# Optimization experiments

Measured on AMD Instinct MI355X. Metric: run time of the kernel, lower is better.

The kernel has to match this reference:

```python
import math
import jax, jax.numpy as jnp
import numpy as np

SEQ_LEN = 512
NUM_HEADS = 16
HEAD_DIM = 64  # hidden_size // num_heads
MAX_REL = 127


def _relative_positions_embeddings(length, depth, max_relative_position=MAX_REL):
    """Sinusoidal table gathered by clipped relative distance -> [L, L, depth]."""
    vocab = 2 * max_relative_position + 1
    pos = np.arange(vocab, dtype=np.float64)[:, None]
    i = np.arange(depth // 2, dtype=np.float64)[None, :]
    angle = pos / np.power(10000.0, 2.0 * i / depth)
    table = np.zeros((vocab, depth), dtype=np.float64)
    table[:, 0::2] = np.sin(angle)
    table[:, 1::2] = np.cos(angle)
    r = np.arange(length)
    dist = np.clip(r[None, :] - r[:, None], -max_relative_position, max_relative_position)
    final = dist + max_relative_position  # [L, L] indices into vocab
    return jnp.asarray(table[final], dtype=jnp.float32)  # [L, L, depth]

_REL_EMB = _relative_positions_embeddings(SEQ_LEN, HEAD_DIM)


def setup_inputs() -> dict:
    key = jax.random.key(0)
    ks = jax.random.split(key, 4)
    B, S, H = 8, SEQ_LEN, NUM_HEADS * HEAD_DIM
    scale = 1.0 / math.sqrt(H)
    return {
        "hidden_states": jax.random.normal(ks[0], (B, S, H), dtype=jnp.float32),
        "attention_mask": jnp.zeros((B, 1, 1, S), dtype=jnp.float32),
        "Wq": jax.random.normal(ks[1], (H, H), dtype=jnp.float32) * scale,
        "bq": jnp.zeros((H,), dtype=jnp.float32),
        "Wk": jax.random.normal(ks[2], (H, H), dtype=jnp.float32) * scale,
        "bk": jnp.zeros((H,), dtype=jnp.float32),
        "Wv": jax.random.normal(ks[3], (H, H), dtype=jnp.float32) * scale,
        "bv": jnp.zeros((H,), dtype=jnp.float32),
    }


def reference(hidden_states, attention_mask, Wq, bq, Wk, bk, Wv, bv):
    B, S, _ = hidden_states.shape
    H, D = NUM_HEADS, HEAD_DIM

    def split_heads(x):  # [B,S,H*D] -> [B,H,S,D]
        return x.reshape(B, S, H, D).transpose(0, 2, 1, 3)

    q = split_heads(hidden_states @ Wq.T + bq)
    k = split_heads(hidden_states @ Wk.T + bk)
    v = split_heads(hidden_states @ Wv.T + bv)

    rel = _REL_EMB[:S, :S, :]  # [S, S, D]

    scores = jnp.einsum("bhqd,bhkd->bhqk", q, k)
    scores = scores + jnp.einsum("bhqd,qkd->bhqk", q, rel)
    scores = scores / math.sqrt(D) + attention_mask

    probs = jax.nn.softmax(scores, axis=-1)  # dropout prob = 0.0 (eval)

    ctx = jnp.einsum("bhqk,bhkd->bhqd", probs, v)
    ctx = ctx + jnp.einsum("bhqk,qkd->bhqd", probs, rel)

    context_layer = ctx.transpose(0, 2, 1, 3).reshape(B, S, H * D)
    return context_layer, scores
```

## Files before the change

### kernel.cpp

```cpp
#include <hip/hip_runtime.h>
#include <hip/hip_bf16.h>

typedef __attribute__((ext_vector_type(4))) float f32x4;
typedef __attribute__((ext_vector_type(8))) short bf16x8;

#define NB 8
#define NS 512
#define NH 16
#define ND 64
#define HID 1024
#define NBH (NB*NH)
#define NROWS (NB*NS)

static __device__ __forceinline__ ushort f2bf(float x){
    union{float f; unsigned u;} a; a.f = x;
    unsigned r = a.u + 0x7fffu + ((a.u >> 16) & 1u);
    return (ushort)(r >> 16);
}
static __device__ __forceinline__ float bf2f(ushort x){
    union{unsigned u; float f;} a; a.u = ((unsigned)x) << 16;
    return a.f;
}

__global__ void build_tables(ushort* __restrict__ tab, ushort* __restrict__ tabT){
    int t = blockIdx.x * blockDim.x + threadIdx.x;
    if (t >= 256 * 64) return;
    int p = t >> 6, d = t & 63;
    float val = 0.f;
    if (p < 255){
        int i = d >> 1;
        float angle = (float)p / powf(10000.f, (float)i / 32.f);
        val = (d & 1) ? cosf(angle) : sinf(angle);
    }
    ushort b = f2bf(val);
    tab[p * 64 + d]  = b;
    tabT[d * 256 + p] = b;
}

__global__ void cvt_bf16(const float* __restrict__ src, ushort* __restrict__ dst, int n4){
    int i = blockIdx.x * blockDim.x + threadIdx.x;
    if (i >= n4) return;
    float4 v = reinterpret_cast<const float4*>(src)[i];
    ushort4 o;
    o.x = f2bf(v.x); o.y = f2bf(v.y); o.z = f2bf(v.z); o.w = f2bf(v.w);
    reinterpret_cast<ushort4*>(dst)[i] = o;
}

__global__ void cvt_bf16_w3(const float* __restrict__ w0, const float* __restrict__ w1,
                            const float* __restrict__ w2, ushort* __restrict__ o0,
                            ushort* __restrict__ o1, ushort* __restrict__ o2, int n4){
    int i = blockIdx.x * blockDim.x + threadIdx.x;
    if (i >= n4) return;
    const float* src = blockIdx.y == 0 ? w0 : (blockIdx.y == 1 ? w1 : w2);
    ushort* dst      = blockIdx.y == 0 ? o0 : (blockIdx.y == 1 ? o1 : o2);
    float4 v = reinterpret_cast<const float4*>(src)[i];
    ushort4 o;
    o.x = f2bf(v.x); o.y = f2bf(v.y); o.z = f2bf(v.z); o.w = f2bf(v.w);
    reinterpret_cast<ushort4*>(dst)[i] = o;
}

__global__ __launch_bounds__(256) void proj_gemm_qkv(
    const ushort* __restrict__ X,
    const ushort* __restrict__ Wqp, const ushort* __restrict__ Wkp, const ushort* __restrict__ Wvp,
    const float* __restrict__ bqp, const float* __restrict__ bkp, const float* __restrict__ bvp,
    ushort* __restrict__ outQ, ushort* __restrict__ outK, ushort* __restrict__ outV)
{
    __shared__ ushort lA[128][72];
    __shared__ ushort lB[128][72];
    int sel = blockIdx.x >> 3;
    const ushort* W   = sel == 0 ? Wqp : (sel == 1 ? Wkp : Wvp);
    const float* bias = sel == 0 ? bqp : (sel == 1 ? bkp : bvp);
    ushort* out       = sel == 0 ? outQ : (sel == 1 ? outK : outV);
    int n0 = (blockIdx.x & 7) * 128;
    int m0 = blockIdx.y * 128;
    int tid = threadIdx.x;
    int wave = tid >> 6, lane = tid & 63;
    int wr = (wave >> 1) * 64, wc = (wave & 1) * 64;
    int lrow = lane & 15, lk8 = (lane >> 4) * 8;

    f32x4 acc[4][4] = {};

    for (int k0 = 0; k0 < HID; k0 += 64){
        __syncthreads();
        #pragma unroll
        for (int i = 0; i < 4; ++i){
            int chunk = i * 256 + tid;
            int row = chunk >> 3, col = (chunk & 7) * 8;
            *reinterpret_cast<uint4*>(&lA[row][col]) =
                *reinterpret_cast<const uint4*>(&X[(size_t)(m0 + row) * HID + k0 + col]);
            *reinterpret_cast<uint4*>(&lB[row][col]) =
                *reinterpret_cast<const uint4*>(&W[(size_t)(n0 + row) * HID + k0 + col]);
        }
        __syncthreads();
        #pragma unroll
        for (int ks = 0; ks < 2; ++ks){
            bf16x8 af[4], bfr[4];
            #pragma unroll
            for (int m = 0; m < 4; ++m)
                af[m] = *reinterpret_cast<const bf16x8*>(&lA[wr + m*16 + lrow][ks*32 + lk8]);
            #pragma unroll
            for (int n = 0; n < 4; ++n)
                bfr[n] = *reinterpret_cast<const bf16x8*>(&lB[wc + n*16 + lrow][ks*32 + lk8]);
            #pragma unroll
            for (int m = 0; m < 4; ++m)
                #pragma unroll
                for (int n = 0; n < 4; ++n)
                    acc[m][n] = __builtin_amdgcn_mfma_f32_16x16x32_bf16(af[m], bfr[n], acc[m][n], 0, 0, 0);
        }
    }

    #pragma unroll
    for (int m = 0; m < 4; ++m){
        #pragma unroll
        for (int n = 0; n < 4; ++n){
            int col = n0 + wc + n*16 + lrow;
            float bv = bias[col];
            int h = col >> 6, d = col & 63;
            #pragma unroll
            for (int r = 0; r < 4; ++r){
                int mg = m0 + wr + m*16 + (lane >> 4)*4 + r;
                int b = mg >> 9, s = mg & 511;
                float val = acc[m][n][r] + bv;
                if (sel != 2)
                    out[(((size_t)(b*NH + h))*NS + s)*ND + d] = f2bf(val);
                else
                    out[(((size_t)(b*NH + h))*ND + d)*NS + s] = f2bf(val);
            }
        }
    }
}

__global__ __launch_bounds__(256, 6) void fused_attn(
    const ushort* __restrict__ Qb, const ushort* __restrict__ Kb,
    const ushort* __restrict__ vT, const ushort* __restrict__ tab,
    const ushort* __restrict__ tabT, const float* __restrict__ mask,
    float* __restrict__ scores, float* __restrict__ ctx)
{
    __shared__ ushort pL[16][512];
    __shared__ ushort qq[16][256];
    __shared__ float  rsum[16][4];
    __shared__ float  rleft[16][4];
    __shared__ float  rright[16][4];
    ushort* pLf = &pL[0][0];
    ushort* qqf = &qq[0][0];
#define SWZ(row, col) ((col) ^ (((row)&7)<<3))

    const int bh = blockIdx.x;
    const int b = bh >> 4, h = bh & 15;
    const int q0 = blockIdx.y * 16;
    const int wave = threadIdx.x >> 6, lane = threadIdx.x & 63;
    const int lrow = lane & 15, g = lane >> 4, lk8 = g * 8;

    const ushort* Qh = Qb + (size_t)bh * NS * ND;
    const ushort* Kh = Kb + (size_t)bh * NS * ND;
    const int q = q0 + lrow;

    bf16x8 qf0 = *reinterpret_cast<const bf16x8*>(&Qh[(size_t)(q0 + lrow)*ND + lk8]);
    bf16x8 qf1 = *reinterpret_cast<const bf16x8*>(&Qh[(size_t)(q0 + lrow)*ND + 32 + lk8]);

    #pragma unroll
    for (int t = 0; t < 4; ++t){
        const ushort* src = &tab[(size_t)(wave*64 + t*16 + lrow)*ND];
        bf16x8 k0v = *reinterpret_cast<const bf16x8*>(&src[lk8]);
        bf16x8 k1v = *reinterpret_cast<const bf16x8*>(&src[32 + lk8]);
        f32x4 at = __builtin_amdgcn_mfma_f32_16x16x32_bf16(k0v, qf0, (f32x4){0.f,0.f,0.f,0.f}, 0, 0, 0);
        at = __builtin_amdgcn_mfma_f32_16x16x32_bf16(k1v, qf1, at, 0, 0, 0);
        ushort4 w;
        w.x = f2bf(at[0]); w.y = f2bf(at[1]); w.z = f2bf(at[2]); w.w = f2bf(at[3]);
        int col = wave*64 + t*16 + g*4;
        *reinterpret_cast<ushort4*>(&qqf[lrow*256 + SWZ(lrow, col)]) = w;
    }
    __syncthreads();

    float st = 0.f, sl = 0.f, sr = 0.f;
    const float* maskb = &mask[b*NS];
    float* srow = &scores[((size_t)bh*NS + q)*NS];
    const ushort* srcK0 = &Kh[(size_t)(wave*128 + lrow)*ND];
    bf16x8 ka = *reinterpret_cast<const bf16x8*>(&srcK0[lk8]);
    bf16x8 kb = *reinterpret_cast<const bf16x8*>(&srcK0[32 + lk8]);
    #pragma unroll
    for (int n = 0; n < 8; ++n){
        bf16x8 ka1, kb1;
        if (n < 7){
            const ushort* s1 = &Kh[(size_t)(wave*128 + (n+1)*16 + lrow)*ND];
            ka1 = *reinterpret_cast<const bf16x8*>(&s1[lk8]);
            kb1 = *reinterpret_cast<const bf16x8*>(&s1[32 + lk8]);
        }
        int kbase = wave*128 + n*16 + g*4;
        f32x4 a = __builtin_amdgcn_mfma_f32_16x16x32_bf16(ka, qf0, (f32x4){0.f,0.f,0.f,0.f}, 0, 0, 0);
        a = __builtin_amdgcn_mfma_f32_16x16x32_bf16(kb, qf1, a, 0, 0, 0);
        float4 mk4 = *reinterpret_cast<const float4*>(&maskb[kbase]);
        float mk[4] = {mk4.x, mk4.y, mk4.z, mk4.w};
        f32x4 sv;
        ushort4 pw;
        #pragma unroll
        for (int r = 0; r < 4; ++r){
            int k = kbase + r;
            int dd = min(127, max(-127, k - q));
            float val = (a[r] + bf2f(qqf[lrow*256 + SWZ(lrow, dd + 127)])) * 0.125f + mk[r];
            sv[r] = val;
            float e = __expf(val);
            st += e;
            if (k <= q - 127) sl += e;
            if (k >= q + 127) sr += e;
            ((ushort*)&pw)[r] = f2bf(e);
        }
        *reinterpret_cast<f32x4*>(&srow[kbase]) = sv;
        *reinterpret_cast<ushort4*>(&pLf[lrow*512 + SWZ(lrow, kbase)]) = pw;
        ka = ka1; kb = kb1;
    }
    st += __shfl_xor(st, 16); st += __shfl_xor(st, 32);
    sl += __shfl_xor(sl, 16); sl += __shfl_xor(sl, 32);
    sr += __shfl_xor(sr, 16); sr += __shfl_xor(sr, 32);
    if (lane < 16){
        rsum[lrow][wave]   = st;
        rleft[lrow][wave]  = sl;
        rright[lrow][wave] = sr;
    }
    __syncthreads();

    if (wave == 0 && lane < 16){
        float SL = rleft[lrow][0] + rleft[lrow][1] + rleft[lrow][2] + rleft[lrow][3];
        float SR = rright[lrow][0] + rright[lrow][1] + rright[lrow][2] + rright[lrow][3];
        qqf[lrow*256 + SWZ(lrow, 0)]   = f2bf(SL);
        qqf[lrow*256 + SWZ(lrow, 254)] = f2bf(SR);
    }
    for (int idx = threadIdx.x; idx < 16*256; idx += 256){
        int row = idx >> 8, j = idx & 255;
        if (j == 0 || j >= 254) continue;
        int col = q0 + row + j - 127;
        qqf[row*256 + SWZ(row, j)] =
            (col >= 0 && col < NS) ? pLf[row*512 + SWZ(row, col)] : (ushort)0;
    }
    __syncthreads();

    const int d = wave*16 + lrow;
    const ushort* vTh = vT + ((size_t)bh*ND + d)*NS;
    const ushort* tTd = tabT + (size_t)d*256;
    f32x4 o0 = (f32x4){0.f,0.f,0.f,0.f};
    f32x4 o1 = (f32x4){0.f,0.f,0.f,0.f};
    __builtin_amdgcn_s_setprio(1);
    #pragma unroll
    for (int k0 = 0; k0 < NS; k0 += 64){
        bf16x8 bv0 = *reinterpret_cast<const bf16x8*>(&vTh[k0 + lk8]);
        bf16x8 pa0 = *reinterpret_cast<const bf16x8*>(&pLf[lrow*512 + SWZ(lrow, k0 + lk8)]);
        o0 = __builtin_amdgcn_mfma_f32_16x16x32_bf16(pa0, bv0, o0, 0, 0, 0);
        bf16x8 bv1 = *reinterpret_cast<const bf16x8*>(&vTh[k0 + 32 + lk8]);
        bf16x8 pa1 = *reinterpret_cast<const bf16x8*>(&pLf[lrow*512 + SWZ(lrow, k0 + 32 + lk8)]);
        o1 = __builtin_amdgcn_mfma_f32_16x16x32_bf16(pa1, bv1, o1, 0, 0, 0);
    }
    #pragma unroll
    for (int k0 = 0; k0 < 256; k0 += 64){
        bf16x8 bv0 = *reinterpret_cast<const bf16x8*>(&tTd[k0 + lk8]);
        bf16x8 pa0 = *reinterpret_cast<const bf16x8*>(&qqf[lrow*256 + SWZ(lrow, k0 + lk8)]);
        o0 = __builtin_amdgcn_mfma_f32_16x16x32_bf16(pa0, bv0, o0, 0, 0, 0);
        bf16x8 bv1 = *reinterpret_cast<const bf16x8*>(&tTd[k0 + 32 + lk8]);
        bf16x8 pa1 = *reinterpret_cast<const bf16x8*>(&qqf[lrow*256 + SWZ(lrow, k0 + 32 + lk8)]);
        o1 = __builtin_amdgcn_mfma_f32_16x16x32_bf16(pa1, bv1, o1, 0, 0, 0);
    }
    __builtin_amdgcn_s_setprio(0);
    #pragma unroll
    for (int r = 0; r < 4; ++r){
        int row = g*4 + r;
        float T = rsum[row][0] + rsum[row][1] + rsum[row][2] + rsum[row][3];
        int qo = q0 + row;
        ctx[((size_t)b*NS + qo)*HID + h*ND + d] = (o0[r] + o1[r]) * (1.f / T);
    }
#undef SWZ
}

extern "C" void kernel_launch(void* const* d_in, const int* in_sizes, int n_in,
                              void* d_out, int out_size, void* d_ws, size_t ws_size,
                              hipStream_t stream)
{
    const float* x    = (const float*)d_in[0];
    const float* mask = (const float*)d_in[1];
    const float* Wq   = (const float*)d_in[2];
    const float* bq   = (const float*)d_in[3];
    const float* Wk   = (const float*)d_in[4];
    const float* bk   = (const float*)d_in[5];
    const float* Wv   = (const float*)d_in[6];
    const float* bv   = (const float*)d_in[7];

    float* out = (float*)d_out;
    float* ctx    = out;
    float* scores = out + (size_t)NB*NS*HID;

    char* ws = (char*)d_ws;
    ushort* x_bf  = (ushort*)ws;  ws += (size_t)NROWS*HID*2;
    ushort* wq_bf = (ushort*)ws;  ws += (size_t)HID*HID*2;
    ushort* wk_bf = (ushort*)ws;  ws += (size_t)HID*HID*2;
    ushort* wv_bf = (ushort*)ws;  ws += (size_t)HID*HID*2;
    ushort* q_bf  = (ushort*)ws;  ws += (size_t)NBH*NS*ND*2;
    ushort* k_bf  = (ushort*)ws;  ws += (size_t)NBH*NS*ND*2;
    ushort* vT_bf = (ushort*)ws;  ws += (size_t)NBH*NS*ND*2;
    ushort* tab   = (ushort*)ws;  ws += 256*64*2;
    ushort* tabT  = (ushort*)ws;  ws += 64*256*2;

    build_tables<<<64, 256, 0, stream>>>(tab, tabT);

    cvt_bf16<<<(NROWS*HID/4 + 255)/256, 256, 0, stream>>>(x, x_bf, NROWS*HID/4);
    cvt_bf16_w3<<<dim3((HID*HID/4 + 255)/256, 3), 256, 0, stream>>>(
        Wq, Wk, Wv, wq_bf, wk_bf, wv_bf, HID*HID/4);

    proj_gemm_qkv<<<dim3(24, 32), 256, 0, stream>>>(
        x_bf, wq_bf, wk_bf, wv_bf, bq, bk, bv, q_bf, k_bf, vT_bf);

    fused_attn<<<dim3(NBH, NS/16), 256, 0, stream>>>(
        q_bf, k_bf, vT_bf, tab, tabT, mask, scores, ctx);
}
```

Baseline: 176.2 us.

## Use direct global-to-LDS async loads with XOR swizzle in QKV projection GEMM

```diff
diff --git a/kernel.cpp b/kernel.cpp
--- a/kernel.cpp
+++ b/kernel.cpp
@@ -20,6 +20,15 @@
 static __device__ __forceinline__ float bf2f(ushort x){
     union{unsigned u; float f;} a; a.u = ((unsigned)x) << 16;
     return a.f;
+}
+
+static __device__ __forceinline__ void async_copy16(const void* gsrc, void* ldst){
+    __builtin_amdgcn_global_load_lds(
+        reinterpret_cast<const __attribute__((address_space(1))) unsigned int*>(
+            reinterpret_cast<uintptr_t>(gsrc)),
+        reinterpret_cast<__attribute__((address_space(3))) unsigned int*>(
+            reinterpret_cast<uintptr_t>(ldst)),
+        16, 0, 0);
 }
 
 __global__ void build_tables(ushort* __restrict__ tab, ushort* __restrict__ tabT){
@@ -65,8 +74,8 @@
     const float* __restrict__ bqp, const float* __restrict__ bkp, const float* __restrict__ bvp,
     ushort* __restrict__ outQ, ushort* __restrict__ outK, ushort* __restrict__ outV)
 {
-    __shared__ ushort lA[128][72];
-    __shared__ ushort lB[128][72];
+    __shared__ ushort lA[128][64];
+    __shared__ ushort lB[128][64];
     int sel = blockIdx.x >> 3;
     const ushort* W   = sel == 0 ? Wqp : (sel == 1 ? Wkp : Wvp);
     const float* bias = sel == 0 ? bqp : (sel == 1 ? bkp : bvp);
@@ -76,20 +85,22 @@
     int tid = threadIdx.x;
     int wave = tid >> 6, lane = tid & 63;
     int wr = (wave >> 1) * 64, wc = (wave & 1) * 64;
-    int lrow = lane & 15, lk8 = (lane >> 4) * 8;
+    int lrow = lane & 15, g = lane >> 4;
+
+    const int srow = tid >> 3;
+    const int gcol = ((tid & 7) ^ (srow & 7)) * 8;
+    char* ldsA = (char*)(&lA[0][0]) + wave * 1024;
+    char* ldsB = (char*)(&lB[0][0]) + wave * 1024;
+    const int sw = lrow & 7;
 
     f32x4 acc[4][4] = {};
 
     for (int k0 = 0; k0 < HID; k0 += 64){
         __syncthreads();
         #pragma unroll
-        for (int i = 0; i < 4; ++i){
-            int chunk = i * 256 + tid;
-            int row = chunk >> 3, col = (chunk & 7) * 8;
-            *reinterpret_cast<uint4*>(&lA[row][col]) =
-                *reinterpret_cast<const uint4*>(&X[(size_t)(m0 + row) * HID + k0 + col]);
-            *reinterpret_cast<uint4*>(&lB[row][col]) =
-                *reinterpret_cast<const uint4*>(&W[(size_t)(n0 + row) * HID + k0 + col]);
+        for (int p = 0; p < 4; ++p){
+            async_copy16(&X[(size_t)(m0 + srow + p*32) * HID + k0 + gcol], ldsA + p*4096);
+            async_copy16(&W[(size_t)(n0 + srow + p*32) * HID + k0 + gcol], ldsB + p*4096);
         }
         __syncthreads();
         #pragma unroll
@@ -97,10 +108,12 @@
             bf16x8 af[4], bfr[4];
             #pragma unroll
             for (int m = 0; m < 4; ++m)
-                af[m] = *reinterpret_cast<const bf16x8*>(&lA[wr + m*16 + lrow][ks*32 + lk8]);
+                af[m] = *reinterpret_cast<const bf16x8*>(
+                    &lA[wr + m*16 + lrow][(((ks*4 + g) ^ sw)) * 8]);
             #pragma unroll
             for (int n = 0; n < 4; ++n)
-                bfr[n] = *reinterpret_cast<const bf16x8*>(&lB[wc + n*16 + lrow][ks*32 + lk8]);
+                bfr[n] = *reinterpret_cast<const bf16x8*>(
+                    &lB[wc + n*16 + lrow][(((ks*4 + g) ^ sw)) * 8]);
             #pragma unroll
             for (int m = 0; m < 4; ++m)
                 #pragma unroll
```

After: 173.6 us, median of 2. No clear change (-1.5%).
